# Optimization experiments

Measured on AMD Instinct MI355X. Metric: run time of the kernel, lower is better.

The kernel has to match this reference:

```python
import jax, jax.numpy as jnp
import numpy as np

DIM = 768
NUM_HEADS = 12
HEAD_DIM = DIM // NUM_HEADS


def setup_inputs() -> dict:
    key = jax.random.key(0)
    k1, k2, k3 = jax.random.split(key, 3)
    B, N, C = 1, 4096, DIM
    x = jax.random.normal(k1, (B, N, C), dtype=jnp.float32)
    w_qkv = jax.random.normal(k2, (C, 3 * C), dtype=jnp.float32) * (C ** -0.5)
    w_proj = jax.random.normal(k3, (C, C), dtype=jnp.float32) * (C ** -0.5)
    b_proj = jnp.zeros((C,), dtype=jnp.float32)
    return {"x": x, "w_qkv": w_qkv, "w_proj": w_proj, "b_proj": b_proj}


def reference(x, w_qkv, w_proj, b_proj):
    B, N, C = x.shape
    H, D = NUM_HEADS, HEAD_DIM
    scale = D ** -0.5
    # QKV projection (no bias), split into heads: [B, N, 3, H, D] -> bhnd
    qkv = (x @ w_qkv).reshape(B, N, 3, H, D)
    qkv = jnp.transpose(qkv, (2, 0, 3, 1, 4))  # [3, B, H, N, D]
    q, k, v = qkv[0], qkv[1], qkv[2]
    # world_size == 1 => all_gather is identity; full attention over N
    attn = jnp.einsum('bhnd,bhmd->bhnm', q * scale, k)
    attn = jax.nn.softmax(attn, axis=-1)
    out = jnp.einsum('bhnm,bhmd->bhnd', attn, v)
    out = jnp.transpose(out, (0, 2, 1, 3)).reshape(B, N, C)
    return out @ w_proj + b_proj
```

## Files before the change

### kernel.cpp

```cpp
#include <hip/hip_runtime.h>
#include <hip/hip_bf16.h>

#define NT 4096
#define CD 768
#define NH 12
#define HD 64
#define CQ 2304

typedef __bf16 bf;
typedef __bf16 v8bf __attribute__((ext_vector_type(8)));
typedef __bf16 v4bf __attribute__((ext_vector_type(4)));
typedef float  v4f  __attribute__((ext_vector_type(4)));

__device__ __forceinline__ void gld16(const bf* g, bf* l) {
  __builtin_amdgcn_global_load_lds(
      (__attribute__((address_space(1))) void*)g,
      (__attribute__((address_space(3))) void*)l,
      16, 0, 0);
}

__device__ __forceinline__ float fexp2(float x) {
#if defined(__HIP_DEVICE_COMPILE__)
  return __builtin_amdgcn_exp2f(x);
#else
  return x;
#endif
}

__global__ __launch_bounds__(256) void prep(
    const float* __restrict__ x, const float* __restrict__ wqkv,
    const float* __restrict__ wproj, bf* __restrict__ Xb,
    bf* __restrict__ WqkvT, bf* __restrict__ WpT) {
  __shared__ float tile[32][33];
  const int b = blockIdx.x, tid = threadIdx.x;
  if (b < 3072) {
    const int i = b * 256 + tid;
    const float4 v = ((const float4*)x)[i];
    bf o4[4] = {(bf)v.x, (bf)v.y, (bf)v.z, (bf)v.w};
    ((ushort4*)Xb)[i] = *(const ushort4*)o4;
    return;
  }
  const float* in;
  bf* out;
  int rows, cols, c0, r0;
  if (b < 4800) {
    const int t = b - 3072;
    in = wqkv; out = WqkvT; rows = CD; cols = CQ;
    c0 = (t % 72) * 32; r0 = (t / 72) * 32;
  } else {
    const int t = b - 4800;
    in = wproj; out = WpT; rows = CD; cols = CD;
    c0 = (t % 24) * 32; r0 = (t / 24) * 32;
  }
  const int tx = tid & 31, ty = tid >> 5;
#pragma unroll
  for (int j = 0; j < 32; j += 8)
    tile[ty + j][tx] = in[(size_t)(r0 + ty + j) * cols + (c0 + tx)];
  __syncthreads();
#pragma unroll
  for (int j = 0; j < 32; j += 8)
    out[(size_t)(c0 + ty + j) * rows + (r0 + tx)] = (bf)tile[tx][ty + j];
}

__global__ __launch_bounds__(256, 3) void gemm_qkv(
    const bf* __restrict__ A, const bf* __restrict__ Bt,
    bf* __restrict__ Qb, bf* __restrict__ Kb, bf* __restrict__ Vtb) {
  __shared__ __align__(16) bf As[128 * 64];
  __shared__ __align__(16) bf Bs[128 * 64];
  const int tid = threadIdx.x;
  const int lane = tid & 63, wave = tid >> 6;
  const int lane15 = lane & 15, quad = lane >> 4;
  const int waveM = wave & 1, waveN = wave >> 1;
  const int bm = blockIdx.x * 128;
  const int bn = blockIdx.y * 128;

  v4f acc[4][4];
#pragma unroll
  for (int i = 0; i < 4; ++i)
#pragma unroll
    for (int j = 0; j < 4; ++j) acc[i][j] = (v4f){0.f, 0.f, 0.f, 0.f};

  for (int k0 = 0; k0 < CD; k0 += 64) {
#pragma unroll
    for (int p = 0; p < 4; ++p) {
      const int t = tid + p * 256;
      const int r = t >> 3, u = t & 7;
      gld16(A + (size_t)(bm + r) * CD + k0 + ((u ^ (r & 7)) << 3), As + t * 8);
    }
#pragma unroll
    for (int p = 0; p < 4; ++p) {
      const int t = tid + p * 256;
      const int r = t >> 3, u = t & 7;
      gld16(Bt + (size_t)(bn + r) * CD + k0 + ((u ^ (r & 7)) << 3), Bs + t * 8);
    }
    asm volatile("s_waitcnt vmcnt(0)" ::: "memory");
    __syncthreads();

    v8bf af[4][2], bfr[4][2];
#pragma unroll
    for (int mt = 0; mt < 4; ++mt) {
      const int rr = waveM * 64 + mt * 16 + lane15;
      const int r7 = rr & 7;
      af[mt][0] = *(const v8bf*)(As + rr * 64 + ((quad ^ r7) << 3));
      af[mt][1] = *(const v8bf*)(As + rr * 64 + (((quad ^ 4) ^ r7) << 3));
    }
#pragma unroll
    for (int nt = 0; nt < 4; ++nt) {
      const int rr = waveN * 64 + nt * 16 + lane15;
      const int r7 = rr & 7;
      bfr[nt][0] = *(const v8bf*)(Bs + rr * 64 + ((quad ^ r7) << 3));
      bfr[nt][1] = *(const v8bf*)(Bs + rr * 64 + (((quad ^ 4) ^ r7) << 3));
    }
#pragma unroll
    for (int mt = 0; mt < 4; ++mt)
#pragma unroll
      for (int nt = 0; nt < 4; ++nt) {
        acc[mt][nt] = __builtin_amdgcn_mfma_f32_16x16x32_bf16(af[mt][0], bfr[nt][0], acc[mt][nt], 0, 0, 0);
        acc[mt][nt] = __builtin_amdgcn_mfma_f32_16x16x32_bf16(af[mt][1], bfr[nt][1], acc[mt][nt], 0, 0, 0);
      }
    __syncthreads();
  }

  const float QSCALE = 0.125f * 1.4426950408889634f;
#pragma unroll
  for (int mt = 0; mt < 4; ++mt) {
    const int rowB = bm + waveM * 64 + mt * 16 + quad * 4;
#pragma unroll
    for (int nt = 0; nt < 4; ++nt) {
      const int col = bn + waveN * 64 + nt * 16 + lane15;
      const int s = col / CD;
      const int rem = col - s * CD;
      const int h = rem >> 6, d = rem & 63;
      if (s == 2) {
        bf vp[4];
#pragma unroll
        for (int i = 0; i < 4; ++i) vp[i] = (bf)acc[mt][nt][i];
        const int pos = (rowB & ~31) + (((rowB & 15) >> 2) << 3) + (((rowB >> 4) & 1) << 2);
        *(uint2*)(Vtb + ((size_t)h * HD + d) * NT + pos) = *(const uint2*)vp;
      } else {
#pragma unroll
        for (int i = 0; i < 4; ++i) {
          const float v = acc[mt][nt][i];
          const int row = rowB + i;
          if (s == 0) Qb[((size_t)h * NT + row) * HD + d] = (bf)(v * QSCALE);
          else        Kb[((size_t)h * NT + row) * HD + d] = (bf)v;
        }
      }
    }
  }
}

__global__ __launch_bounds__(256, 4) void attn(
    const bf* __restrict__ Qb, const bf* __restrict__ Kb,
    const bf* __restrict__ Vtb, bf* __restrict__ Ob) {
  __shared__ __align__(16) char smem[32768];

  const int b = blockIdx.x;
  int h, qt;
  if (b < 512) { h = b & 7;        qt = b >> 3; }
  else { const int bb = b - 512; h = 8 + (bb & 3); qt = bb >> 2; }
  const int q0 = qt * 64;

  const int tid = threadIdx.x;
  const int wave = tid >> 6, lane = tid & 63;
  const int kh = wave & 1;
  const int sh = wave >> 1;
  const int lane15 = lane & 15, quad = lane >> 4;

  const bf* Kh = Kb + (size_t)h * NT * HD;
  const bf* Vh = Vtb + (size_t)h * HD * NT;

  v8bf aQ[2][2];
#pragma unroll
  for (int sl = 0; sl < 2; ++sl) {
    const int qrow = q0 + (sh * 2 + sl) * 16 + lane15;
    aQ[sl][0] = *(const v8bf*)(Qb + ((size_t)h * NT + qrow) * HD + quad * 8);
    aQ[sl][1] = *(const v8bf*)(Qb + ((size_t)h * NT + qrow) * HD + 32 + quad * 8);
  }

  v4f o[2][4];
#pragma unroll
  for (int sl = 0; sl < 2; ++sl)
#pragma unroll
    for (int dt = 0; dt < 4; ++dt) o[sl][dt] = (v4f){0.f, 0.f, 0.f, 0.f};
  v4f den[2] = {(v4f){0.f, 0.f, 0.f, 0.f}, (v4f){0.f, 0.f, 0.f, 0.f}};
  v8bf vone;
#pragma unroll
  for (int i = 0; i < 8; ++i) vone[i] = (bf)1.0f;

  auto stage = [&](int half, int kt) {
    bf* Kdst = (bf*)(smem + half * 16384);
    bf* Vdst = (bf*)(smem + half * 16384 + 8192);
#pragma unroll
    for (int p = 0; p < 2; ++p) {
      const int L = p * 256 + tid;
      const int r = L >> 3, u = L & 7;
      gld16(Kh + (size_t)(kt + r) * HD + ((u ^ (r & 7)) << 3), Kdst + L * 8);
    }
#pragma unroll
    for (int p = 0; p < 2; ++p) {
      const int L = p * 256 + tid;
      const int d = L >> 3, u = L & 7;
      gld16(Vh + (size_t)d * NT + kt + ((u ^ (d & 7)) << 3), Vdst + L * 8);
    }
  };

  stage(0, 0);
  asm volatile("s_waitcnt vmcnt(0)" ::: "memory");
  __syncthreads();

  for (int it = 0; it < NT / 64; ++it) {
    const int half = it & 1;
    if (it + 1 < NT / 64) stage(half ^ 1, (it + 1) * 64);

    const bf* Kbuf = (const bf*)(smem + half * 16384);
    const bf* Vbuf = (const bf*)(smem + half * 16384 + 8192);

    v8bf aP8[2];
#pragma unroll
    for (int e = 0; e < 2; ++e) {
      const int k = kh * 32 + e * 16 + lane15;
      const int k7 = k & 7;
      const v8bf bk0 = *(const v8bf*)(Kbuf + k * 64 + ((quad ^ k7) << 3));
      const v8bf bk1 = *(const v8bf*)(Kbuf + k * 64 + (((quad ^ 4) ^ k7) << 3));
#pragma unroll
      for (int sl = 0; sl < 2; ++sl) {
        v4f z = (v4f){0.f, 0.f, 0.f, 0.f};
        __builtin_amdgcn_s_setprio(1);
        z = __builtin_amdgcn_mfma_f32_16x16x32_bf16(bk0, aQ[sl][0], z, 0, 0, 0);
        z = __builtin_amdgcn_mfma_f32_16x16x32_bf16(bk1, aQ[sl][1], z, 0, 0, 0);
        __builtin_amdgcn_s_setprio(0);
#pragma unroll
        for (int r = 0; r < 4; ++r) aP8[sl][e * 4 + r] = (bf)fexp2(z[r]);
      }
    }

#pragma unroll
    for (int sl = 0; sl < 2; ++sl)
      den[sl] = __builtin_amdgcn_mfma_f32_16x16x32_bf16(aP8[sl], vone, den[sl], 0, 0, 0);
#pragma unroll
    for (int dt = 0; dt < 4; ++dt) {
      const int d = dt * 16 + lane15;
      const v8bf bv = *(const v8bf*)(Vbuf + d * 64 + (((kh * 4 + quad) ^ (d & 7)) << 3));
      __builtin_amdgcn_s_setprio(1);
#pragma unroll
      for (int sl = 0; sl < 2; ++sl)
        o[sl][dt] = __builtin_amdgcn_mfma_f32_16x16x32_bf16(aP8[sl], bv, o[sl][dt], 0, 0, 0);
      __builtin_amdgcn_s_setprio(0);
    }

    asm volatile("s_waitcnt vmcnt(0)" ::: "memory");
    __syncthreads();
  }

  float* Red = (float*)smem;
  float* Ls  = (float*)(smem + 16384);
#pragma unroll
  for (int sl = 0; sl < 2; ++sl) {
    __syncthreads();
    float* reg = Red + wave * 1024;
#pragma unroll
    for (int dt = 0; dt < 4; ++dt)
      *(v4f*)(reg + dt * 256 + lane15 * 16 + quad * 4) = o[sl][dt];
    if (lane15 == 0) {
#pragma unroll
      for (int i = 0; i < 4; ++i) Ls[wave * 16 + quad * 4 + i] = den[sl][i];
    }
    __syncthreads();
    const int s = sh * 2 + sl;
    const float dsum = Ls[(sh * 2) * 16 + lane15] + Ls[(sh * 2 + 1) * 16 + lane15];
    const float linv = 1.f / dsum;
#pragma unroll
    for (int dh = 0; dh < 2; ++dh) {
      const int dt = kh * 2 + dh;
      v4f sum = *(const v4f*)(Red + (sh * 2) * 1024 + dt * 256 + lane15 * 16 + quad * 4);
      sum     += *(const v4f*)(Red + (sh * 2 + 1) * 1024 + dt * 256 + lane15 * 16 + quad * 4);
#pragma unroll
      for (int i = 0; i < 4; ++i) {
        const float linv_i = __shfl(linv, quad * 4 + i, 64);
        const int row = q0 + s * 16 + quad * 4 + i;
        Ob[(size_t)row * CD + h * HD + dt * 16 + lane15] = (bf)(sum[i] * linv_i);
      }
    }
  }
}

__global__ __launch_bounds__(256, 4) void gemm_proj(
    const bf* __restrict__ A, const bf* __restrict__ Bt,
    const float* __restrict__ bias, float* __restrict__ out) {
  __shared__ __align__(16) bf As[2][64 * 32];
  __shared__ __align__(16) bf Bs[2][128 * 32];
  const int tid = threadIdx.x;
  const int lane = tid & 63, wave = tid >> 6;
  const int lane15 = lane & 15, quad = lane >> 4;
  const int bm = blockIdx.x * 64;
  const int bn = blockIdx.y * 128;

  v4f acc[4][2];
#pragma unroll
  for (int i = 0; i < 4; ++i)
#pragma unroll
    for (int j = 0; j < 2; ++j) acc[i][j] = (v4f){0.f, 0.f, 0.f, 0.f};

  auto stageG = [&](int half, int k0) {
    {
      const int r = tid >> 2, c = (tid & 3) * 8;
      gld16(A + (size_t)(bm + r) * CD + k0 + c, As[half] + tid * 8);
    }
#pragma unroll
    for (int p = 0; p < 2; ++p) {
      const int t = tid + p * 256;
      const int r = t >> 2, c = (t & 3) * 8;
      gld16(Bt + (size_t)(bn + r) * CD + k0 + c, Bs[half] + t * 8);
    }
  };

  stageG(0, 0);
  asm volatile("s_waitcnt vmcnt(0)" ::: "memory");
  __syncthreads();

  for (int it = 0; it < CD / 32; ++it) {
    const int half = it & 1;
    if (it + 1 < CD / 32) stageG(half ^ 1, (it + 1) * 32);

    v8bf af[4], bfr[2];
#pragma unroll
    for (int mt = 0; mt < 4; ++mt)
      af[mt] = *(const v8bf*)(As[half] + (mt * 16 + lane15) * 32 + quad * 8);
#pragma unroll
    for (int nt = 0; nt < 2; ++nt)
      bfr[nt] = *(const v8bf*)(Bs[half] + (wave * 32 + nt * 16 + lane15) * 32 + quad * 8);
#pragma unroll
    for (int mt = 0; mt < 4; ++mt)
#pragma unroll
      for (int nt = 0; nt < 2; ++nt)
        acc[mt][nt] = __builtin_amdgcn_mfma_f32_16x16x32_bf16(af[mt], bfr[nt], acc[mt][nt], 0, 0, 0);

    asm volatile("s_waitcnt vmcnt(0)" ::: "memory");
    __syncthreads();
  }

#pragma unroll
  for (int mt = 0; mt < 4; ++mt) {
    const int rowB = bm + mt * 16 + quad * 4;
#pragma unroll
    for (int nt = 0; nt < 2; ++nt) {
      const int col = bn + wave * 32 + nt * 16 + lane15;
      const float bcol = bias[col];
#pragma unroll
      for (int i = 0; i < 4; ++i)
        out[(size_t)(rowB + i) * CD + col] = acc[mt][nt][i] + bcol;
    }
  }
}

extern "C" void kernel_launch(void* const* d_in, const int* in_sizes, int n_in,
                              void* d_out, int out_size, void* d_ws, size_t ws_size,
                              hipStream_t stream) {
  const float* x     = (const float*)d_in[0];
  const float* wqkv  = (const float*)d_in[1];
  const float* wproj = (const float*)d_in[2];
  const float* bproj = (const float*)d_in[3];
  float* out = (float*)d_out;

  bf* ws    = (bf*)d_ws;
  bf* Xb    = ws;  ws += (size_t)NT * CD;
  bf* WqkvT = ws;  ws += (size_t)CQ * CD;
  bf* WpT   = ws;  ws += (size_t)CD * CD;
  bf* Qb    = ws;  ws += (size_t)NH * NT * HD;
  bf* Kb    = ws;  ws += (size_t)NH * NT * HD;
  bf* Vtb   = ws;  ws += (size_t)NH * NT * HD;
  bf* Ob    = ws;  ws += (size_t)NT * CD;

  prep<<<5376, 256, 0, stream>>>(x, wqkv, wproj, Xb, WqkvT, WpT);
  gemm_qkv<<<dim3(NT / 128, CQ / 128), 256, 0, stream>>>(Xb, WqkvT, Qb, Kb, Vtb);
  attn<<<768, 256, 0, stream>>>(Qb, Kb, Vtb, Ob);
  gemm_proj<<<dim3(NT / 64, CD / 128), 256, 0, stream>>>(Ob, WpT, bproj, out);
}
```

Baseline: 173.1 us.

## Load K tiles directly into registers and stage only V through LDS

The attention loop no longer copies K tiles into shared memory. Each wave loads its own K fragments from global memory straight into registers, double-buffered across an unrolled pair of iterations, while V still goes through a double-buffered LDS ring that is now half the size. This removes the K LDS write and read traffic and shrinks shared memory per block. Occupancy hints drop from 4 to 3 blocks, and the direct global loads of K are smaller and less coalesced, which adds register pressure and load latency.

```diff
diff --git a/kernel.cpp b/kernel.cpp
--- a/kernel.cpp
+++ b/kernel.cpp
@@ -150,10 +150,10 @@
   }
 }
 
-__global__ __launch_bounds__(256, 4) void attn(
+__global__ __launch_bounds__(256, 3) void attn(
     const bf* __restrict__ Qb, const bf* __restrict__ Kb,
     const bf* __restrict__ Vtb, bf* __restrict__ Ob) {
-  __shared__ __align__(16) char smem[32768];
+  __shared__ __align__(16) char smem[16640];
 
   const int b = blockIdx.x;
   int h, qt;
@@ -188,15 +188,20 @@
 #pragma unroll
   for (int i = 0; i < 8; ++i) vone[i] = (bf)1.0f;
 
-  auto stage = [&](int half, int kt) {
-    bf* Kdst = (bf*)(smem + half * 16384);
-    bf* Vdst = (bf*)(smem + half * 16384 + 8192);
-#pragma unroll
-    for (int p = 0; p < 2; ++p) {
-      const int L = p * 256 + tid;
-      const int r = L >> 3, u = L & 7;
-      gld16(Kh + (size_t)(kt + r) * HD + ((u ^ (r & 7)) << 3), Kdst + L * 8);
-    }
+  const bf* Kl0 = Kh + (size_t)(kh * 32 + lane15) * HD + quad * 8;
+  const bf* Kl1 = Kh + (size_t)(kh * 32 + 16 + lane15) * HD + quad * 8;
+
+  auto loadK = [&](v8bf (&kr)[2][2], int kt) {
+    const bf* p0 = Kl0 + (size_t)kt * HD;
+    const bf* p1 = Kl1 + (size_t)kt * HD;
+    kr[0][0] = *(const v8bf*)(p0);
+    kr[0][1] = *(const v8bf*)(p0 + 32);
+    kr[1][0] = *(const v8bf*)(p1);
+    kr[1][1] = *(const v8bf*)(p1 + 32);
+  };
+
+  auto stageV = [&](int half, int kt) {
+    bf* Vdst = (bf*)(smem + half * 8192);
 #pragma unroll
     for (int p = 0; p < 2; ++p) {
       const int L = p * 256 + tid;
@@ -205,36 +210,22 @@
     }
   };
 
-  stage(0, 0);
-  asm volatile("s_waitcnt vmcnt(0)" ::: "memory");
-  __syncthreads();
-
-  for (int it = 0; it < NT / 64; ++it) {
-    const int half = it & 1;
-    if (it + 1 < NT / 64) stage(half ^ 1, (it + 1) * 64);
-
-    const bf* Kbuf = (const bf*)(smem + half * 16384);
-    const bf* Vbuf = (const bf*)(smem + half * 16384 + 8192);
-
+  auto computeT = [&](int half, v8bf (&kr)[2][2]) {
+    const bf* Vbuf = (const bf*)(smem + half * 8192);
     v8bf aP8[2];
 #pragma unroll
     for (int e = 0; e < 2; ++e) {
-      const int k = kh * 32 + e * 16 + lane15;
-      const int k7 = k & 7;
-      const v8bf bk0 = *(const v8bf*)(Kbuf + k * 64 + ((quad ^ k7) << 3));
-      const v8bf bk1 = *(const v8bf*)(Kbuf + k * 64 + (((quad ^ 4) ^ k7) << 3));
 #pragma unroll
       for (int sl = 0; sl < 2; ++sl) {
         v4f z = (v4f){0.f, 0.f, 0.f, 0.f};
         __builtin_amdgcn_s_setprio(1);
-        z = __builtin_amdgcn_mfma_f32_16x16x32_bf16(bk0, aQ[sl][0], z, 0, 0, 0);
-        z = __builtin_amdgcn_mfma_f32_16x16x32_bf16(bk1, aQ[sl][1], z, 0, 0, 0);
+        z = __builtin_amdgcn_mfma_f32_16x16x32_bf16(kr[e][0], aQ[sl][0], z, 0, 0, 0);
+        z = __builtin_amdgcn_mfma_f32_16x16x32_bf16(kr[e][1], aQ[sl][1], z, 0, 0, 0);
         __builtin_amdgcn_s_setprio(0);
 #pragma unroll
         for (int r = 0; r < 4; ++r) aP8[sl][e * 4 + r] = (bf)fexp2(z[r]);
       }
     }
-
 #pragma unroll
     for (int sl = 0; sl < 2; ++sl)
       den[sl] = __builtin_amdgcn_mfma_f32_16x16x32_bf16(aP8[sl], vone, den[sl], 0, 0, 0);
@@ -248,7 +239,27 @@
         o[sl][dt] = __builtin_amdgcn_mfma_f32_16x16x32_bf16(aP8[sl], bv, o[sl][dt], 0, 0, 0);
       __builtin_amdgcn_s_setprio(0);
     }
-
+  };
+
+  v8bf kA[2][2], kB[2][2];
+  loadK(kA, 0);
+  stageV(0, 0);
+  asm volatile("s_waitcnt vmcnt(0)" ::: "memory");
+  __syncthreads();
+
+#pragma unroll 1
+  for (int it2 = 0; it2 < 32; ++it2) {
+    const int it = it2 * 2;
+    stageV(1, (it + 1) * 64);
+    loadK(kB, (it + 1) * 64);
+    computeT(0, kA);
+    asm volatile("s_waitcnt vmcnt(0)" ::: "memory");
+    __syncthreads();
+    if (it + 2 < 64) {
+      stageV(0, (it + 2) * 64);
+      loadK(kA, (it + 2) * 64);
+    }
+    computeT(1, kB);
     asm volatile("s_waitcnt vmcnt(0)" ::: "memory");
     __syncthreads();
   }
```

Result: slower. 210.0 us (+21.3%).
